# Performance work log

Measured on AMD Instinct MI355X. Metric: run time of the kernel, lower is better.

The kernel has to match this reference:

```python
import jax, jax.numpy as jnp
import numpy as np

# DREAMPlace IDXST_IDCT (a.k.a. idsct2): y[u,v] = sum_p sum_q x[p,q] * sin(pi*p*(u+0.5)/M) * cos(pi*q*(v+0.5)/N)
# i.e. IDXST (inverse discrete sine transform, DST-III-like, unnormalized) along the M axis
# and IDCT (DCT-III-like, unnormalized, full weight on k=0) along the N axis.
# Computed with the classic 2N-padded FFT trick using the precomputed twiddles
# expk[k] = exp(-1j*pi*k/(2N)) stored as [N,2] (real, imag), matching precompute_expk.

def _idxt_spectrum(x, expk):
    """F[u] = sum_k x[k] * exp(-1j*pi*k*(2u+1)/(2N)), along last axis.
    Re(F) is the IDCT sum (cos), -Im(F) is the IDXST sum (sin)."""
    N = x.shape[-1]
    c = (x * expk[..., 0]) + 1j * (x * expk[..., 1])  # x[k] * exp(-j*pi*k/(2N))
    z = jnp.concatenate([c, jnp.zeros_like(c)], axis=-1)  # zero-pad to 2N
    return jnp.fft.fft(z, axis=-1)[..., :N]


def idct_1d(x, expk):
    # y[u] = sum_k x[k] cos(pi*k*(2u+1)/(2N))
    return _idxt_spectrum(x, expk).real


def idxst_1d(x, expk):
    # y[u] = sum_k x[k] sin(pi*k*(2u+1)/(2N))
    return -_idxt_spectrum(x, expk).imag


def _make_expk(L):
    k = jnp.arange(L, dtype=jnp.float32) * (np.pi / (2.0 * L))
    return jnp.stack([jnp.cos(k), -jnp.sin(k)], axis=-1)  # exp(-j*pi*k/(2L))


def setup_inputs() -> dict:
    M, N = 4096, 4096
    key = jax.random.key(0)
    x = jax.random.normal(key, (M, N), dtype=jnp.float32)
    return {"x": x, "expkM": _make_expk(M), "expkN": _make_expk(N)}


def reference(x, expkM, expkN):
    # IDCT along the last dim (N), then IDXST along the second-to-last dim (M):
    # idxst(idct(x)^T)^T
    t = idct_1d(x, expkN)                                        # [M, N]
    y = idxst_1d(t.swapaxes(-2, -1), expkM).swapaxes(-2, -1)     # [M, N]
    return y
```

## Files before the change

### kernel.cpp

```cpp
#include <hip/hip_runtime.h>
#include <hip/hip_bf16.h>
#include <stdint.h>
#include <cmath>


typedef __attribute__((ext_vector_type(4))) float f32x4;
typedef __attribute__((ext_vector_type(8))) unsigned short u16x8;
typedef __attribute__((ext_vector_type(8))) __bf16 bf16x8;

__device__ __forceinline__ unsigned short f2bf(float f) {
  union { float f; unsigned u; } v; v.f = f;
  unsigned u = v.u + 0x7fffu + ((v.u >> 16) & 1u);
  return (unsigned short)(u >> 16);
}
__device__ __forceinline__ float bf2f(unsigned short h) {
  union { unsigned u; float f; } v; v.u = ((unsigned)h) << 16;
  return v.f;
}

__device__ __forceinline__ void gen_half(int idx, u16x8* Pe, u16x8* Po,
                                         int isSin, int jshift, int jmask,
                                         unsigned mask4L, float sc) {
  int i = idx >> jshift;
  int jb = (idx & jmask) * 8;
  unsigned tp = 2u * (unsigned)i + 1u;
  unsigned re = (2u * (unsigned)jb * tp) & mask4L;
  unsigned ro = (re + tp) & mask4L;
  unsigned step = (2u * tp) & mask4L;
  u16x8 pe, po;
#pragma unroll
  for (int t = 0; t < 8; t++) {
    float se_, ce_, so_, co_;
    __sincosf((float)re * sc, &se_, &ce_);
    __sincosf((float)ro * sc, &so_, &co_);
    pe[t] = f2bf(isSin ? se_ : ce_);
    po[t] = f2bf(isSin ? so_ : co_);
    re = (re + step) & mask4L;
    ro = (ro + step) & mask4L;
  }
  Pe[idx] = pe;
  Po[idx] = po;
}

__global__ void prep_kernel(const f32x4* __restrict__ x, u16x8* __restrict__ xe,
                            u16x8* __restrict__ xo, u16x8* __restrict__ Ce,
                            u16x8* __restrict__ Co, u16x8* __restrict__ Se,
                            u16x8* __restrict__ So, int nConvBlocks,
                            int nGenNBlocks, int jshiftN, int jmaskN,
                            unsigned mask4N, float scN, int jshiftM, int jmaskM,
                            unsigned mask4M, float scM) {
  int b = blockIdx.x;
  if (b < nConvBlocks) {
    int idx = b * 256 + threadIdx.x;
    f32x4 a = x[4 * idx], bb = x[4 * idx + 1], c = x[4 * idx + 2],
          d = x[4 * idx + 3];
    u16x8 e, o;
    e[0] = f2bf(a[0]);  o[0] = f2bf(a[1]);  e[1] = f2bf(a[2]);  o[1] = f2bf(a[3]);
    e[2] = f2bf(bb[0]); o[2] = f2bf(bb[1]); e[3] = f2bf(bb[2]); o[3] = f2bf(bb[3]);
    e[4] = f2bf(c[0]);  o[4] = f2bf(c[1]);  e[5] = f2bf(c[2]);  o[5] = f2bf(c[3]);
    e[6] = f2bf(d[0]);  o[6] = f2bf(d[1]);  e[7] = f2bf(d[2]);  o[7] = f2bf(d[3]);
    xe[idx] = e;
    xo[idx] = o;
  } else if (b < nConvBlocks + nGenNBlocks) {
    int idx = (b - nConvBlocks) * 256 + threadIdx.x;
    gen_half(idx, Ce, Co, 0, jshiftN, jmaskN, mask4N, scN);
  } else {
    int idx = (b - nConvBlocks - nGenNBlocks) * 256 + threadIdx.x;
    gen_half(idx, Se, So, 1, jshiftM, jmaskM, mask4M, scM);
  }
}

template <bool OUT_BF16>
__global__ __launch_bounds__(256, 2) void btgemm_kernel(
    const unsigned short* __restrict__ A0,
    const unsigned short* __restrict__ A1,
    const unsigned short* __restrict__ B0,
    const unsigned short* __restrict__ B1,
    void* __restrict__ C0v, void* __restrict__ C1v, int Ndim, int K) {
  __shared__ unsigned short As[128 * 32];
  __shared__ unsigned short Bs[128 * 32];

  const unsigned short* A = blockIdx.z ? A1 : A0;
  const unsigned short* Bt = blockIdx.z ? B1 : B0;
  void* C = blockIdx.z ? C1v : C0v;

  const int tid = threadIdx.x;
  const int m0 = blockIdx.y * 128;
  const int n0 = blockIdx.x * 128;

  const int wave = tid >> 6;
  const int lane = tid & 63;
  const int wm = (wave & 1) * 64;
  const int wn = (wave >> 1) * 64;
  const int l16 = lane & 15;
  const int quad = lane >> 4;

  f32x4 acc[4][4];
#pragma unroll
  for (int i = 0; i < 4; i++)
#pragma unroll
    for (int j = 0; j < 4; j++) acc[i][j] = f32x4{0.f, 0.f, 0.f, 0.f};

  const int rs0 = wave * 16 + (lane >> 2);
  const int rs1 = 64 + rs0;
  const int cs = (lane & 3) * 8;
  const unsigned short* Ag0 = A + (size_t)(m0 + rs0) * K + cs;
  const unsigned short* Ag1 = A + (size_t)(m0 + rs1) * K + cs;
  const unsigned short* Bg0 = Bt + (size_t)(n0 + rs0) * K + cs;
  const unsigned short* Bg1 = Bt + (size_t)(n0 + rs1) * K + cs;
  unsigned short* Al0 = As + wave * 512;
  unsigned short* Al1 = As + 2048 + wave * 512;
  unsigned short* Bl0 = Bs + wave * 512;
  unsigned short* Bl1 = Bs + 2048 + wave * 512;

  for (int k0 = 0; k0 < K; k0 += 32) {
    __builtin_amdgcn_global_load_lds(
        (const __attribute__((address_space(1))) void*)(Ag0 + k0),
        (__attribute__((address_space(3))) void*)Al0, 16, 0, 0);
    __builtin_amdgcn_global_load_lds(
        (const __attribute__((address_space(1))) void*)(Ag1 + k0),
        (__attribute__((address_space(3))) void*)Al1, 16, 0, 0);
    __builtin_amdgcn_global_load_lds(
        (const __attribute__((address_space(1))) void*)(Bg0 + k0),
        (__attribute__((address_space(3))) void*)Bl0, 16, 0, 0);
    __builtin_amdgcn_global_load_lds(
        (const __attribute__((address_space(1))) void*)(Bg1 + k0),
        (__attribute__((address_space(3))) void*)Bl1, 16, 0, 0);
    __syncthreads();

    bf16x8 af[4], bfr[4];
#pragma unroll
    for (int i = 0; i < 4; i++) {
      af[i]  = *(const bf16x8*)(As + (wm + i * 16 + l16) * 32 + quad * 8);
      bfr[i] = *(const bf16x8*)(Bs + (wn + i * 16 + l16) * 32 + quad * 8);
    }
#pragma unroll
    for (int i = 0; i < 4; i++)
#pragma unroll
      for (int j = 0; j < 4; j++)
        acc[i][j] = __builtin_amdgcn_mfma_f32_16x16x32_bf16(af[i], bfr[j],
                                                            acc[i][j], 0, 0, 0);
    __syncthreads();
  }

#pragma unroll
  for (int i = 0; i < 4; i++) {
#pragma unroll
    for (int j = 0; j < 4; j++) {
      int col = n0 + wn + j * 16 + l16;
      int rowb = m0 + wm + i * 16 + quad * 4;
#pragma unroll
      for (int r = 0; r < 4; r++) {
        float v = acc[i][j][r];
        if (OUT_BF16)
          ((unsigned short*)C)[(size_t)(rowb + r) * Ndim + col] = f2bf(v);
        else
          ((float*)C)[(size_t)(rowb + r) * Ndim + col] = v;
      }
    }
  }
}

__global__ void bfly1_kernel(const u16x8* __restrict__ E1,
                             const u16x8* __restrict__ O1,
                             u16x8* __restrict__ tTe, u16x8* __restrict__ tTo,
                             int pshift, int pmask, int Nrows, int Mh8) {
  int idx = blockIdx.x * blockDim.x + threadIdx.x;
  int v = idx >> pshift;
  int pu = idx & pmask;
  u16x8 e0 = E1[2 * idx], e1 = E1[2 * idx + 1];
  u16x8 o0 = O1[2 * idx], o1 = O1[2 * idx + 1];
  u16x8 tet, tot, teb, tob;
#pragma unroll
  for (int k = 0; k < 4; k++) {
    float ee = bf2f(e0[2 * k]), eo = bf2f(e0[2 * k + 1]);
    float oe = bf2f(o0[2 * k]), oo = bf2f(o0[2 * k + 1]);
    tet[k] = f2bf(ee + oe); tot[k] = f2bf(eo + oo);
    teb[k] = f2bf(ee - oe); tob[k] = f2bf(eo - oo);
  }
#pragma unroll
  for (int k = 0; k < 4; k++) {
    float ee = bf2f(e1[2 * k]), eo = bf2f(e1[2 * k + 1]);
    float oe = bf2f(o1[2 * k]), oo = bf2f(o1[2 * k + 1]);
    tet[4 + k] = f2bf(ee + oe); tot[4 + k] = f2bf(eo + oo);
    teb[4 + k] = f2bf(ee - oe); tob[4 + k] = f2bf(eo - oo);
  }
  tTe[idx] = tet;
  tTo[idx] = tot;
  int idxb = (Nrows - 1 - v) * Mh8 + pu;
  tTe[idxb] = teb;
  tTo[idxb] = tob;
}

__global__ void bfly2_kernel(const f32x4* __restrict__ E2,
                             const f32x4* __restrict__ O2,
                             f32x4* __restrict__ y, int vshift, int vmask,
                             int Mrows, int N4) {
  int idx = blockIdx.x * blockDim.x + threadIdx.x;
  int u = idx >> vshift;
  int vu = (idx & vmask) * 4;
  int baseb = (Mrows - 1 - u) * N4 + vu;
  int baset = u * N4 + vu;
#pragma unroll
  for (int t = 0; t < 4; t++) {
    f32x4 e = E2[4 * idx + t];
    f32x4 o = O2[4 * idx + t];
    y[baset + t] = e + o;
    y[baseb + t] = o - e;
  }
}

extern "C" void kernel_launch(void* const* d_in, const int* in_sizes, int n_in,
                              void* d_out, int out_size, void* d_ws,
                              size_t ws_size, hipStream_t stream) {
  const float* x = (const float*)d_in[0];
  const int M = in_sizes[1] / 2;
  const int N = in_sizes[2] / 2;
  const size_t MN = (size_t)M * N;

  unsigned short* ws = (unsigned short*)d_ws;
  unsigned short* xe = ws;
  unsigned short* xo = ws + MN / 2;
  unsigned short* tTe = ws + MN;
  unsigned short* tTo = ws + MN * 3 / 2;
  unsigned short* Ce = ws + MN * 2;
  unsigned short* Co = ws + MN * 2 + MN / 4;
  unsigned short* Se = ws + MN * 5 / 2;
  unsigned short* So = ws + MN * 5 / 2 + MN / 4;
  unsigned short* E1 = ws + MN * 3;
  unsigned short* O1 = ws + MN * 7 / 2;
  float* E2 = (float*)ws;
  float* O2 = (float*)(ws + MN * 3);

  int shiftN = 0; while ((1 << shiftN) < N) shiftN++;
  int shiftM = 0; while ((1 << shiftM) < M) shiftM++;

  int nConvBlocks = (int)(MN / 16 / 256);
  int nGenNBlocks = (N / 2) * (N / 2) / 8 / 256;
  int nGenMBlocks = (M / 2) * (M / 2) / 8 / 256;
  prep_kernel<<<nConvBlocks + nGenNBlocks + nGenMBlocks, 256, 0, stream>>>(
      (const f32x4*)x, (u16x8*)xe, (u16x8*)xo, (u16x8*)Ce, (u16x8*)Co,
      (u16x8*)Se, (u16x8*)So, nConvBlocks, nGenNBlocks, shiftN - 4,
      (N / 16) - 1, (unsigned)(4 * N - 1),
      (float)(3.14159265358979323846 / (2.0 * N)), shiftM - 4, (M / 16) - 1,
      (unsigned)(4 * M - 1), (float)(3.14159265358979323846 / (2.0 * M)));

  btgemm_kernel<true><<<dim3(M / 128, (N / 2) / 128, 2), 256, 0, stream>>>(
      Ce, Co, xe, xo, E1, O1, M, N / 2);

  bfly1_kernel<<<(int)(MN / 32 / 256), 256, 0, stream>>>(
      (const u16x8*)E1, (const u16x8*)O1, (u16x8*)tTe, (u16x8*)tTo, shiftM - 4,
      (M / 16) - 1, N, M / 16);

  btgemm_kernel<false><<<dim3(N / 128, (M / 2) / 128, 2), 256, 0, stream>>>(
      Se, So, tTe, tTo, E2, O2, N, M / 2);

  bfly2_kernel<<<(int)(MN / 32 / 256), 256, 0, stream>>>(
      (const f32x4*)E2, (const f32x4*)O2, (f32x4*)d_out, shiftN - 4,
      (N / 16) - 1, M, N / 4);
}
```

Baseline: 320.1 us.

## Double GEMM K-tile to 64 with XOR-swizzled LDS and bf16 second-stage output

The GEMM kernel now stages a 64-wide K slice per iteration instead of 32. LDS rows are XOR-swizzled to avoid bank conflicts, and two MFMA sub-steps run per barrier pair, which halves the synchronisation count. The second GEMM now writes bf16 intermediates instead of fp32, halving that write and the butterfly read; the final butterfly widens back to fp32. The workspace layout is reshuffled so E2/O2 reuse the xe/xo buffers. This adds rounding error from the bf16 intermediate, and doubled LDS use may affect occupancy.

```diff
diff --git a/kernel.cpp b/kernel.cpp
--- a/kernel.cpp
+++ b/kernel.cpp
@@ -70,19 +70,19 @@
   }
 }
 
-template <bool OUT_BF16>
 __global__ __launch_bounds__(256, 2) void btgemm_kernel(
     const unsigned short* __restrict__ A0,
     const unsigned short* __restrict__ A1,
     const unsigned short* __restrict__ B0,
     const unsigned short* __restrict__ B1,
-    void* __restrict__ C0v, void* __restrict__ C1v, int Ndim, int K) {
-  __shared__ unsigned short As[128 * 32];
-  __shared__ unsigned short Bs[128 * 32];
+    unsigned short* __restrict__ C0, unsigned short* __restrict__ C1, int Ndim,
+    int K) {
+  __shared__ unsigned short As[128 * 64];
+  __shared__ unsigned short Bs[128 * 64];
 
   const unsigned short* A = blockIdx.z ? A1 : A0;
   const unsigned short* Bt = blockIdx.z ? B1 : B0;
-  void* C = blockIdx.z ? C1v : C0v;
+  unsigned short* C = blockIdx.z ? C1 : C0;
 
   const int tid = threadIdx.x;
   const int m0 = blockIdx.y * 128;
@@ -101,45 +101,51 @@
 #pragma unroll
     for (int j = 0; j < 4; j++) acc[i][j] = f32x4{0.f, 0.f, 0.f, 0.f};
 
-  const int rs0 = wave * 16 + (lane >> 2);
-  const int rs1 = 64 + rs0;
-  const int cs = (lane & 3) * 8;
-  const unsigned short* Ag0 = A + (size_t)(m0 + rs0) * K + cs;
-  const unsigned short* Ag1 = A + (size_t)(m0 + rs1) * K + cs;
-  const unsigned short* Bg0 = Bt + (size_t)(n0 + rs0) * K + cs;
-  const unsigned short* Bg1 = Bt + (size_t)(n0 + rs1) * K + cs;
-  unsigned short* Al0 = As + wave * 512;
-  unsigned short* Al1 = As + 2048 + wave * 512;
-  unsigned short* Bl0 = Bs + wave * 512;
-  unsigned short* Bl1 = Bs + 2048 + wave * 512;
-
-  for (int k0 = 0; k0 < K; k0 += 32) {
-    __builtin_amdgcn_global_load_lds(
-        (const __attribute__((address_space(1))) void*)(Ag0 + k0),
-        (__attribute__((address_space(3))) void*)Al0, 16, 0, 0);
-    __builtin_amdgcn_global_load_lds(
-        (const __attribute__((address_space(1))) void*)(Ag1 + k0),
-        (__attribute__((address_space(3))) void*)Al1, 16, 0, 0);
-    __builtin_amdgcn_global_load_lds(
-        (const __attribute__((address_space(1))) void*)(Bg0 + k0),
-        (__attribute__((address_space(3))) void*)Bl0, 16, 0, 0);
-    __builtin_amdgcn_global_load_lds(
-        (const __attribute__((address_space(1))) void*)(Bg1 + k0),
-        (__attribute__((address_space(3))) void*)Bl1, 16, 0, 0);
+  const int lrow = lane >> 3;
+  const int lsw = ((lane & 7) ^ lrow) * 8;
+  const unsigned short* Ag[4];
+  const unsigned short* Bg[4];
+  unsigned short* Al[4];
+  unsigned short* Bl[4];
+#pragma unroll
+  for (int t = 0; t < 4; t++) {
+    int ch = wave + 4 * t;
+    Ag[t] = A + (size_t)(m0 + 8 * ch + lrow) * K + lsw;
+    Bg[t] = Bt + (size_t)(n0 + 8 * ch + lrow) * K + lsw;
+    Al[t] = As + ch * 512;
+    Bl[t] = Bs + ch * 512;
+  }
+
+  const int swz = (quad ^ (l16 & 7)) * 8;
+
+  for (int k0 = 0; k0 < K; k0 += 64) {
+#pragma unroll
+    for (int t = 0; t < 4; t++) {
+      __builtin_amdgcn_global_load_lds(
+          (const __attribute__((address_space(1))) void*)(Ag[t] + k0),
+          (__attribute__((address_space(3))) void*)Al[t], 16, 0, 0);
+      __builtin_amdgcn_global_load_lds(
+          (const __attribute__((address_space(1))) void*)(Bg[t] + k0),
+          (__attribute__((address_space(3))) void*)Bl[t], 16, 0, 0);
+    }
     __syncthreads();
 
-    bf16x8 af[4], bfr[4];
-#pragma unroll
-    for (int i = 0; i < 4; i++) {
-      af[i]  = *(const bf16x8*)(As + (wm + i * 16 + l16) * 32 + quad * 8);
-      bfr[i] = *(const bf16x8*)(Bs + (wn + i * 16 + l16) * 32 + quad * 8);
-    }
-#pragma unroll
-    for (int i = 0; i < 4; i++)
-#pragma unroll
-      for (int j = 0; j < 4; j++)
-        acc[i][j] = __builtin_amdgcn_mfma_f32_16x16x32_bf16(af[i], bfr[j],
-                                                            acc[i][j], 0, 0, 0);
+#pragma unroll
+    for (int h = 0; h < 2; h++) {
+      const int so = swz ^ (h * 32);
+      bf16x8 af[4], bfr[4];
+#pragma unroll
+      for (int i = 0; i < 4; i++) {
+        af[i]  = *(const bf16x8*)(As + (wm + i * 16 + l16) * 64 + so);
+        bfr[i] = *(const bf16x8*)(Bs + (wn + i * 16 + l16) * 64 + so);
+      }
+#pragma unroll
+      for (int i = 0; i < 4; i++)
+#pragma unroll
+        for (int j = 0; j < 4; j++)
+          acc[i][j] = __builtin_amdgcn_mfma_f32_16x16x32_bf16(
+              af[i], bfr[j], acc[i][j], 0, 0, 0);
+    }
     __syncthreads();
   }
 
@@ -150,13 +156,8 @@
       int col = n0 + wn + j * 16 + l16;
       int rowb = m0 + wm + i * 16 + quad * 4;
 #pragma unroll
-      for (int r = 0; r < 4; r++) {
-        float v = acc[i][j][r];
-        if (OUT_BF16)
-          ((unsigned short*)C)[(size_t)(rowb + r) * Ndim + col] = f2bf(v);
-        else
-          ((float*)C)[(size_t)(rowb + r) * Ndim + col] = v;
-      }
+      for (int r = 0; r < 4; r++)
+        C[(size_t)(rowb + r) * Ndim + col] = f2bf(acc[i][j][r]);
     }
   }
 }
@@ -192,21 +193,42 @@
   tTo[idxb] = tob;
 }
 
-__global__ void bfly2_kernel(const f32x4* __restrict__ E2,
-                             const f32x4* __restrict__ O2,
+__global__ void bfly2_kernel(const u16x8* __restrict__ E2,
+                             const u16x8* __restrict__ O2,
                              f32x4* __restrict__ y, int vshift, int vmask,
                              int Mrows, int N4) {
   int idx = blockIdx.x * blockDim.x + threadIdx.x;
   int u = idx >> vshift;
   int vu = (idx & vmask) * 4;
+  u16x8 e0 = E2[2 * idx], e1 = E2[2 * idx + 1];
+  u16x8 o0 = O2[2 * idx], o1 = O2[2 * idx + 1];
+  int baset = u * N4 + vu;
   int baseb = (Mrows - 1 - u) * N4 + vu;
-  int baset = u * N4 + vu;
-#pragma unroll
-  for (int t = 0; t < 4; t++) {
-    f32x4 e = E2[4 * idx + t];
-    f32x4 o = O2[4 * idx + t];
-    y[baset + t] = e + o;
-    y[baseb + t] = o - e;
+#pragma unroll
+  for (int t = 0; t < 2; t++) {
+    f32x4 tv, bv;
+#pragma unroll
+    for (int k = 0; k < 4; k++) {
+      float e = bf2f(e0[t * 4 + k]);
+      float o = bf2f(o0[t * 4 + k]);
+      tv[k] = e + o;
+      bv[k] = o - e;
+    }
+    y[baset + t] = tv;
+    y[baseb + t] = bv;
+  }
+#pragma unroll
+  for (int t = 0; t < 2; t++) {
+    f32x4 tv, bv;
+#pragma unroll
+    for (int k = 0; k < 4; k++) {
+      float e = bf2f(e1[t * 4 + k]);
+      float o = bf2f(o1[t * 4 + k]);
+      tv[k] = e + o;
+      bv[k] = o - e;
+    }
+    y[baset + 2 + t] = tv;
+    y[baseb + 2 + t] = bv;
   }
 }
 
@@ -221,16 +243,16 @@
   unsigned short* ws = (unsigned short*)d_ws;
   unsigned short* xe = ws;
   unsigned short* xo = ws + MN / 2;
-  unsigned short* tTe = ws + MN;
-  unsigned short* tTo = ws + MN * 3 / 2;
-  unsigned short* Ce = ws + MN * 2;
-  unsigned short* Co = ws + MN * 2 + MN / 4;
-  unsigned short* Se = ws + MN * 5 / 2;
-  unsigned short* So = ws + MN * 5 / 2 + MN / 4;
-  unsigned short* E1 = ws + MN * 3;
-  unsigned short* O1 = ws + MN * 7 / 2;
-  float* E2 = (float*)ws;
-  float* O2 = (float*)(ws + MN * 3);
+  unsigned short* Ce = ws + MN;
+  unsigned short* Co = ws + MN + MN / 4;
+  unsigned short* Se = ws + MN * 3 / 2;
+  unsigned short* So = ws + MN * 7 / 4;
+  unsigned short* E1 = ws + MN * 2;
+  unsigned short* O1 = ws + MN * 5 / 2;
+  unsigned short* tTe = ws + MN * 3;
+  unsigned short* tTo = ws + MN * 7 / 2;
+  unsigned short* E2 = xe;
+  unsigned short* O2 = xo;
 
   int shiftN = 0; while ((1 << shiftN) < N) shiftN++;
   int shiftM = 0; while ((1 << shiftM) < M) shiftM++;
@@ -245,17 +267,17 @@
       (float)(3.14159265358979323846 / (2.0 * N)), shiftM - 4, (M / 16) - 1,
       (unsigned)(4 * M - 1), (float)(3.14159265358979323846 / (2.0 * M)));
 
-  btgemm_kernel<true><<<dim3(M / 128, (N / 2) / 128, 2), 256, 0, stream>>>(
+  btgemm_kernel<<<dim3(M / 128, (N / 2) / 128, 2), 256, 0, stream>>>(
       Ce, Co, xe, xo, E1, O1, M, N / 2);
 
   bfly1_kernel<<<(int)(MN / 32 / 256), 256, 0, stream>>>(
       (const u16x8*)E1, (const u16x8*)O1, (u16x8*)tTe, (u16x8*)tTo, shiftM - 4,
       (M / 16) - 1, N, M / 16);
 
-  btgemm_kernel<false><<<dim3(N / 128, (M / 2) / 128, 2), 256, 0, stream>>>(
+  btgemm_kernel<<<dim3(N / 128, (M / 2) / 128, 2), 256, 0, stream>>>(
       Se, So, tTe, tTo, E2, O2, N, M / 2);
 
   bfly2_kernel<<<(int)(MN / 32 / 256), 256, 0, stream>>>(
-      (const f32x4*)E2, (const f32x4*)O2, (f32x4*)d_out, shiftN - 4,
+      (const u16x8*)E2, (const u16x8*)O2, (f32x4*)d_out, shiftN - 4,
       (N / 16) - 1, M, N / 4);
 }
```

Result: faster. 282.3 us (-11.8%).
